# Kernel optimization log

Measured on AMD Instinct MI355X. Metric: run time of the kernel, lower is better.

The kernel has to match this reference:

```python
import jax, jax.numpy as jnp
import numpy as np

DIM = 1024
HEADS = 16
DIM_HEAD = 64
INNER = HEADS * DIM_HEAD  # 1024
SCALE = DIM_HEAD ** -0.5


def setup_inputs() -> dict:
    key = jax.random.key(0)
    k0, k1, k2 = jax.random.split(key, 3)
    x = jax.random.normal(k0, (4, 2048, DIM), dtype=jnp.float32)
    ln_gamma = jnp.ones((DIM,), dtype=jnp.float32)
    ln_beta = jnp.zeros((DIM,), dtype=jnp.float32)
    w_qkv = jax.random.normal(k1, (DIM, 3 * INNER), dtype=jnp.float32) * (DIM ** -0.5)
    w_out = jax.random.normal(k2, (INNER, DIM), dtype=jnp.float32) * (INNER ** -0.5)
    b_out = jnp.zeros((DIM,), dtype=jnp.float32)
    return {"x": x, "ln_gamma": ln_gamma, "ln_beta": ln_beta,
            "w_qkv": w_qkv, "w_out": w_out, "b_out": b_out}


def reference(x, ln_gamma, ln_beta, w_qkv, w_out, b_out):
    # LayerNorm over last dim (eps matches torch default 1e-5)
    mu = jnp.mean(x, axis=-1, keepdims=True)
    var = jnp.mean(jnp.square(x - mu), axis=-1, keepdims=True)
    xn = (x - mu) * jax.lax.rsqrt(var + 1e-5) * ln_gamma + ln_beta
    # QKV projection (no bias)
    qkv = xn @ w_qkv  # [b, t, 3*inner]
    q, k, v = jnp.split(qkv, 3, axis=-1)
    B, T, _ = x.shape
    def to_heads(t):
        return t.reshape(B, T, HEADS, DIM_HEAD).transpose(0, 2, 1, 3)  # b h t d
    q, k, v = to_heads(q), to_heads(k), to_heads(v)
    dots = jnp.einsum('bhid,bhjd->bhij', q, k) * SCALE
    attn = jax.nn.softmax(dots, axis=-1)
    out = jnp.einsum('bhij,bhjd->bhid', attn, v)
    out = out.transpose(0, 2, 1, 3).reshape(B, T, INNER)
    return out @ w_out + b_out
```

## Files before the change

kernel.cpp:

```cpp
#include <hip/hip_runtime.h>


#define DIMX 1024
#define TSEQ 2048
#define NB 4
#define NH 16
#define DH 64
#define NROWS (NB * TSEQ)
#define QSCALE 0.18033688011112042f

typedef __bf16 bf16_t;
typedef __bf16 bf16x8 __attribute__((ext_vector_type(8)));
typedef __bf16 bf16x4 __attribute__((ext_vector_type(4)));
typedef float f32x4 __attribute__((ext_vector_type(4)));

#if __has_builtin(__builtin_amdgcn_exp2f)
#define EXP2F __builtin_amdgcn_exp2f
#else
#define EXP2F exp2f
#endif

__device__ __forceinline__ bf16x4 cvt4(f32x4 v) {
    return __builtin_convertvector(v, bf16x4);
}
__device__ __forceinline__ void async16(const bf16_t* g, bf16_t* l) {
    __builtin_amdgcn_global_load_lds(
        (const __attribute__((address_space(1))) unsigned int*)g,
        (__attribute__((address_space(3))) unsigned int*)l, 16, 0, 0);
}

__global__ __launch_bounds__(256) void ln_kernel(
    const float* __restrict__ x, const float* __restrict__ g,
    const float* __restrict__ b, bf16_t* __restrict__ xn) {
    int row = blockIdx.x, tid = threadIdx.x;
    const float4 xv = *(const float4*)(x + (size_t)row * DIMX + tid * 4);
    float s = xv.x + xv.y + xv.z + xv.w;
    float q = xv.x * xv.x + xv.y * xv.y + xv.z * xv.z + xv.w * xv.w;
    for (int o = 32; o > 0; o >>= 1) {
        s += __shfl_xor(s, o);
        q += __shfl_xor(q, o);
    }
    __shared__ float2 red[4];
    int wave = tid >> 6, lane = tid & 63;
    if (lane == 0) red[wave] = make_float2(s, q);
    __syncthreads();
    float2 r0 = red[0], r1 = red[1], r2 = red[2], r3 = red[3];
    s = r0.x + r1.x + r2.x + r3.x;
    q = r0.y + r1.y + r2.y + r3.y;
    float mu = s * (1.0f / DIMX);
    float var = q * (1.0f / DIMX) - mu * mu;
    float rstd = rsqrtf(var + 1e-5f);
    float4 gv = *(const float4*)(g + tid * 4);
    float4 bv = *(const float4*)(b + tid * 4);
    f32x4 r;
    r[0] = (xv.x - mu) * rstd * gv.x + bv.x;
    r[1] = (xv.y - mu) * rstd * gv.y + bv.y;
    r[2] = (xv.z - mu) * rstd * gv.z + bv.z;
    r[3] = (xv.w - mu) * rstd * gv.w + bv.w;
    *(bf16x4*)(xn + (size_t)row * DIMX + tid * 4) = cvt4(r);
}

__global__ __launch_bounds__(256) void transpose_cast(
    const float* __restrict__ src, bf16_t* __restrict__ dst, int R, int C) {
    __shared__ float tile[32][33];
    int c0 = blockIdx.x * 32, r0 = blockIdx.y * 32;
    int tx = threadIdx.x, ty = threadIdx.y;
    for (int i = ty; i < 32; i += 8)
        tile[i][tx] = src[(size_t)(r0 + i) * C + c0 + tx];
    __syncthreads();
    for (int i = ty; i < 32; i += 8)
        dst[(size_t)(c0 + i) * R + r0 + tx] = (bf16_t)tile[tx][i];
}

#define MFMA16 __builtin_amdgcn_mfma_f32_16x16x32_bf16

template <int MODE>
__global__ __launch_bounds__(256, 2) void gemm128p(
    const bf16_t* __restrict__ A, const bf16_t* __restrict__ BT,
    void* __restrict__ Cout, const float* __restrict__ bias, int M, int N, int K) {
    __shared__ __align__(16) bf16_t As[2][128 * 64];
    __shared__ __align__(16) bf16_t Bs[2][128 * 64];
    int tid = threadIdx.x, lane = tid & 63, wave = tid >> 6;
    int lm = lane & 15, quad = lane >> 4;
    int wr = wave >> 1, wc = wave & 1;

    int nbx = gridDim.x;
    int nwg = nbx * gridDim.y;
    int linear = blockIdx.y * nbx + blockIdx.x;
    int cpx = nwg >> 3;
    int swz = (linear & 7) * cpx + (linear >> 3);
    int bx = swz % nbx, by = swz / nbx;
    int m0 = by * 128, n0 = bx * 128;

    int srow = tid >> 3, sc8 = tid & 7;
    int scol = (sc8 ^ (srow & 7)) << 3;
    const bf16_t* ga = A + (size_t)(m0 + srow) * K + scol;
    const bf16_t* gb = BT + (size_t)(n0 + srow) * K + scol;
    int ldst = tid << 3;

    int sw0 = ((quad ^ (lm & 7)) << 3);
    int sw1 = (((4 + quad) ^ (lm & 7)) << 3);

    f32x4 zero = {0.f, 0.f, 0.f, 0.f};
    f32x4 acc[4][4];
#pragma unroll
    for (int i = 0; i < 4; ++i)
#pragma unroll
        for (int j = 0; j < 4; ++j) acc[i][j] = zero;

#pragma unroll
    for (int i = 0; i < 4; ++i) async16(ga + (size_t)(i * 32) * K, &As[0][i * 2048 + ldst]);
#pragma unroll
    for (int i = 0; i < 4; ++i) async16(gb + (size_t)(i * 32) * K, &Bs[0][i * 2048 + ldst]);
    asm volatile("s_waitcnt vmcnt(0)" ::: "memory");
    __builtin_amdgcn_s_barrier();

    int nkt = K >> 6;
    for (int kt = 0; kt < nkt; ++kt) {
        int c = kt & 1;
        int k1 = (kt + 1) << 6;
        bool pf = (kt + 1) < nkt;
        const bf16_t* pa = &As[c][0];
        const bf16_t* pb = &Bs[c][0];
        bf16_t* na = &As[c ^ 1][0];
        bf16_t* nb = &Bs[c ^ 1][0];
        bf16x8 af[4][2], bfr[2][2];

#pragma unroll
        for (int t = 0; t < 4; ++t) {
            int ro = (wr * 64 + t * 16 + lm) * 64;
            af[t][0] = *(const bf16x8*)&pa[ro + sw0];
            af[t][1] = *(const bf16x8*)&pa[ro + sw1];
        }
#pragma unroll
        for (int t = 0; t < 2; ++t) {
            int ro = (wc * 64 + t * 16 + lm) * 64;
            bfr[t][0] = *(const bf16x8*)&pb[ro + sw0];
            bfr[t][1] = *(const bf16x8*)&pb[ro + sw1];
        }
        if (pf) {
#pragma unroll
            for (int i = 0; i < 4; ++i)
                async16(ga + (size_t)(i * 32) * K + k1, &na[i * 2048 + ldst]);
#pragma unroll
            for (int i = 0; i < 4; ++i)
                async16(gb + (size_t)(i * 32) * K + k1, &nb[i * 2048 + ldst]);
        }
        __builtin_amdgcn_s_barrier();
        asm volatile("s_waitcnt lgkmcnt(0)" ::: "memory");
        __builtin_amdgcn_s_setprio(1);
#pragma unroll
        for (int mt = 0; mt < 4; ++mt)
#pragma unroll
            for (int nt = 0; nt < 2; ++nt) {
                acc[mt][nt] = MFMA16(af[mt][0], bfr[nt][0], acc[mt][nt], 0, 0, 0);
                acc[mt][nt] = MFMA16(af[mt][1], bfr[nt][1], acc[mt][nt], 0, 0, 0);
            }
        __builtin_amdgcn_s_setprio(0);
        __builtin_amdgcn_s_barrier();

#pragma unroll
        for (int t = 0; t < 2; ++t) {
            int ro = (wc * 64 + (2 + t) * 16 + lm) * 64;
            bfr[t][0] = *(const bf16x8*)&pb[ro + sw0];
            bfr[t][1] = *(const bf16x8*)&pb[ro + sw1];
        }
        __builtin_amdgcn_s_barrier();
        asm volatile("s_waitcnt lgkmcnt(0)" ::: "memory");
        __builtin_amdgcn_s_setprio(1);
#pragma unroll
        for (int mt = 0; mt < 4; ++mt)
#pragma unroll
            for (int nt = 0; nt < 2; ++nt) {
                acc[mt][2 + nt] = MFMA16(af[mt][0], bfr[nt][0], acc[mt][2 + nt], 0, 0, 0);
                acc[mt][2 + nt] = MFMA16(af[mt][1], bfr[nt][1], acc[mt][2 + nt], 0, 0, 0);
            }
        __builtin_amdgcn_s_setprio(0);
        asm volatile("s_waitcnt vmcnt(0)" ::: "memory");
        __builtin_amdgcn_s_barrier();
    }

#pragma unroll
    for (int mt = 0; mt < 4; ++mt) {
#pragma unroll
        for (int nt = 0; nt < 4; ++nt) {
            int m = m0 + wr * 64 + mt * 16 + quad * 4;
            int n = n0 + wc * 64 + nt * 16 + lm;
            if (MODE == 1) {
                int sel = n >> 10, nn = n & 1023, h = nn >> 6, d = nn & 63;
                int b = m >> 11, t = m & 2047;
                if (sel == 2) {
                    *(bf16x4*)((bf16_t*)Cout + (size_t)2 * 8388608 +
                               ((size_t)((b * NH + h) * DH + d)) * TSEQ + t) = cvt4(acc[mt][nt]);
                } else {
                    f32x4 sv = acc[mt][nt] * (sel == 0 ? QSCALE : 1.0f);
                    bf16x4 c4 = cvt4(sv);
#pragma unroll
                    for (int r = 0; r < 4; ++r)
                        ((bf16_t*)Cout)[(size_t)sel * 8388608 +
                                        ((size_t)((b * NH + h) * TSEQ + t + r)) * DH + d] = c4[r];
                }
            } else {
                float bn = bias[n];
#pragma unroll
                for (int r = 0; r < 4; ++r)
                    ((float*)Cout)[(size_t)(m + r) * N + n] = acc[mt][nt][r] + bn;
            }
        }
    }
}

__global__ __launch_bounds__(512, 4) void attn_mfma(
    const bf16_t* __restrict__ qkv, bf16_t* __restrict__ o) {
    int bh = blockIdx.y;
    int qt = blockIdx.x;
    const bf16_t* qb = qkv + (size_t)bh * TSEQ * DH;
    const bf16_t* kb = qkv + (size_t)8388608 + (size_t)bh * TSEQ * DH;
    const bf16_t* vb = qkv + (size_t)16777216 + (size_t)bh * DH * TSEQ;
    int tid = threadIdx.x, wave = tid >> 6, lane = tid & 63;
    int lm = lane & 15, quad = lane >> 4, lx = lm & 7;

    __shared__ __align__(16) bf16_t Ks[2][2][64 * 64];
    __shared__ __align__(16) bf16_t Vt[2][2][64 * 64];

    int roff = tid >> 3;
    int fr = (roff & 3) | ((roff & 8) >> 1);
    int cperm = ((tid & 7) ^ fr) * 8;
    const bf16_t* kp = kb + (size_t)roff * DH + cperm;
    const bf16_t* vp = vb + (size_t)roff * TSEQ + cperm;
    int l0 = tid * 8;

    bf16x8 qf[2][2];
#pragma unroll
    for (int u = 0; u < 2; ++u)
#pragma unroll
        for (int ks = 0; ks < 2; ++ks)
            qf[u][ks] = *(const bf16x8*)(qb +
                (size_t)(qt * 256 + wave * 32 + u * 16 + lm) * DH + ks * 32 + quad * 8);

    f32x4 zero = {0.f, 0.f, 0.f, 0.f};
    f32x4 m16 = {-16.f, -16.f, -16.f, -16.f};
    f32x4 acc[2][4];
#pragma unroll
    for (int u = 0; u < 2; ++u)
#pragma unroll
        for (int dt = 0; dt < 4; ++dt) acc[u][dt] = zero;
    f32x4 l4[2] = {zero, zero};

    int qh = lm >> 2, rr = lm & 3;
    int krow0 = 8 * qh + rr;
    int krow1 = krow0 + 4;
    int krow2 = 32 + 8 * (qh ^ 2) + rr;
    int krow3 = krow2 + 4;
    int fo0 = (quad ^ lx) * 8;
    int fo1 = ((4 + quad) ^ lx) * 8;
    int fv = (lm & 3) | ((lm & 8) >> 1);
    int vo0 = (quad ^ fv) * 8;
    int vo1 = ((4 | (quad ^ 2)) ^ fv) * 8;

    async16(kp, &Ks[0][0][l0]);
    async16(kp + (size_t)64 * DH, &Ks[0][1][l0]);
    async16(vp, &Vt[0][0][l0]);
    async16(vp + 64, &Vt[0][1][l0]);
    kp += 128 * DH; vp += 128;
    asm volatile("s_waitcnt vmcnt(0)" ::: "memory");
    __builtin_amdgcn_s_barrier();

    for (int jt = 0; jt < TSEQ / 128; ++jt) {
        int c = jt & 1;
        if (jt + 1 < TSEQ / 128) {
            async16(kp, &Ks[c ^ 1][0][l0]);
            async16(kp + (size_t)64 * DH, &Ks[c ^ 1][1][l0]);
            async16(vp, &Vt[c ^ 1][0][l0]);
            async16(vp + 64, &Vt[c ^ 1][1][l0]);
            kp += 128 * DH; vp += 128;
        }

#pragma unroll
        for (int sub = 0; sub < 2; ++sub) {
            const bf16_t* Kc = &Ks[c][sub][0];
            const bf16_t* Vc = &Vt[c][sub][0];

            bf16x8 kf[4][2];
            kf[0][0] = *(const bf16x8*)&Kc[krow0 * 64 + fo0];
            kf[0][1] = *(const bf16x8*)&Kc[krow0 * 64 + fo1];
            kf[1][0] = *(const bf16x8*)&Kc[krow1 * 64 + fo0];
            kf[1][1] = *(const bf16x8*)&Kc[krow1 * 64 + fo1];
            kf[2][0] = *(const bf16x8*)&Kc[krow2 * 64 + fo0];
            kf[2][1] = *(const bf16x8*)&Kc[krow2 * 64 + fo1];
            kf[3][0] = *(const bf16x8*)&Kc[krow3 * 64 + fo0];
            kf[3][1] = *(const bf16x8*)&Kc[krow3 * 64 + fo1];

            bf16x8 pf[2][2];
#pragma unroll
            for (int u = 0; u < 2; ++u) {
                f32x4 s[4];
                __builtin_amdgcn_s_setprio(1);
#pragma unroll
                for (int nt = 0; nt < 4; ++nt) {
                    s[nt] = __builtin_amdgcn_mfma_f32_16x16x32_bf16(kf[nt][0], qf[u][0], m16, 0, 0, 0);
                    s[nt] = __builtin_amdgcn_mfma_f32_16x16x32_bf16(kf[nt][1], qf[u][1], s[nt], 0, 0, 0);
                }
                __builtin_amdgcn_s_setprio(0);
                f32x4 p[4];
#pragma unroll
                for (int nt = 0; nt < 4; ++nt) {
#pragma unroll
                    for (int e = 0; e < 4; ++e) p[nt][e] = EXP2F(s[nt][e]);
                    l4[u] += p[nt];
                }
                bf16x4 c0 = cvt4(p[0]), c1 = cvt4(p[1]), c2 = cvt4(p[2]), c3 = cvt4(p[3]);
                pf[u][0] = __builtin_shufflevector(c0, c1, 0, 1, 2, 3, 4, 5, 6, 7);
                pf[u][1] = __builtin_shufflevector(c2, c3, 0, 1, 2, 3, 4, 5, 6, 7);
            }

            __builtin_amdgcn_s_setprio(1);
#pragma unroll
            for (int dt = 0; dt < 4; ++dt) {
                bf16x8 vf0 = *(const bf16x8*)&Vc[(dt * 16 + lm) * 64 + vo0];
                bf16x8 vf1 = *(const bf16x8*)&Vc[(dt * 16 + lm) * 64 + vo1];
#pragma unroll
                for (int u = 0; u < 2; ++u) {
                    acc[u][dt] = __builtin_amdgcn_mfma_f32_16x16x32_bf16(vf0, pf[u][0], acc[u][dt], 0, 0, 0);
                    acc[u][dt] = __builtin_amdgcn_mfma_f32_16x16x32_bf16(vf1, pf[u][1], acc[u][dt], 0, 0, 0);
                }
            }
            __builtin_amdgcn_s_setprio(0);
        }

        asm volatile("s_waitcnt vmcnt(0)" ::: "memory");
        __builtin_amdgcn_s_barrier();
    }

    int b = bh >> 4, h = bh & 15;
#pragma unroll
    for (int u = 0; u < 2; ++u) {
        float l = (l4[u][0] + l4[u][1]) + (l4[u][2] + l4[u][3]);
        l += __shfl_xor(l, 16);
        l += __shfl_xor(l, 32);
        float rl = 1.0f / l;
        int t = qt * 256 + wave * 32 + u * 16 + lm;
#pragma unroll
        for (int dt = 0; dt < 4; ++dt) {
            f32x4 ov = acc[u][dt] * rl;
            *(bf16x4*)(o + ((size_t)(b * TSEQ + t)) * DIMX + h * DH + dt * 16 + quad * 4) = cvt4(ov);
        }
    }
}

extern "C" void kernel_launch(void* const* d_in, const int* in_sizes, int n_in,
                              void* d_out, int out_size, void* d_ws, size_t ws_size,
                              hipStream_t stream) {
    const float* x = (const float*)d_in[0];
    const float* g = (const float*)d_in[1];
    const float* be = (const float*)d_in[2];
    const float* w_qkv = (const float*)d_in[3];
    const float* w_out = (const float*)d_in[4];
    const float* b_out = (const float*)d_in[5];
    float* out = (float*)d_out;
    char* ws = (char*)d_ws;

    bf16_t* xn = (bf16_t*)(ws);
    bf16_t* wqkvT = (bf16_t*)(ws + 16777216);
    bf16_t* woutT = (bf16_t*)(ws + 23068672);
    bf16_t* qkv = (bf16_t*)(ws + 25165824);
    bf16_t* attno = (bf16_t*)(ws + 75497472);

    ln_kernel<<<NROWS, 256, 0, stream>>>(x, g, be, xn);
    transpose_cast<<<dim3(96, 32), dim3(32, 8), 0, stream>>>(w_qkv, wqkvT, 1024, 3072);
    transpose_cast<<<dim3(32, 32), dim3(32, 8), 0, stream>>>(w_out, woutT, 1024, 1024);
    gemm128p<1><<<dim3(24, 64), 256, 0, stream>>>(xn, wqkvT, (void*)qkv, nullptr, NROWS, 3072, 1024);
    attn_mfma<<<dim3(8, 64), 512, 0, stream>>>(qkv, attno);
    gemm128p<2><<<dim3(8, 64), 256, 0, stream>>>(attno, woutT, (void*)out, b_out, NROWS, 1024, 1024);
}
```

Baseline: 262.3 us.

## Merge LayerNorm and weight transposes into one kernel; load all B fragments at once

Fuses the LayerNorm kernel and the two weight transpose-cast kernels into a single prep kernel launch, dispatching work by block index. This removes two kernel launches and the gaps between them. In the GEMM main loop, all four B fragments are now read from LDS up front and all 16 MFMA pairs are issued in one phase. This drops the mid-iteration barriers and the second LDS read stage, at the cost of more registers held live and less interleaving of LDS reads with MFMA.

```diff
diff --git a/kernel.cpp b/kernel.cpp
--- a/kernel.cpp
+++ b/kernel.cpp
@@ -29,47 +29,58 @@
         (__attribute__((address_space(3))) unsigned int*)l, 16, 0, 0);
 }
 
-__global__ __launch_bounds__(256) void ln_kernel(
+__global__ __launch_bounds__(256) void prep_kernel(
     const float* __restrict__ x, const float* __restrict__ g,
-    const float* __restrict__ b, bf16_t* __restrict__ xn) {
-    int row = blockIdx.x, tid = threadIdx.x;
-    const float4 xv = *(const float4*)(x + (size_t)row * DIMX + tid * 4);
-    float s = xv.x + xv.y + xv.z + xv.w;
-    float q = xv.x * xv.x + xv.y * xv.y + xv.z * xv.z + xv.w * xv.w;
-    for (int o = 32; o > 0; o >>= 1) {
-        s += __shfl_xor(s, o);
-        q += __shfl_xor(q, o);
-    }
-    __shared__ float2 red[4];
-    int wave = tid >> 6, lane = tid & 63;
-    if (lane == 0) red[wave] = make_float2(s, q);
-    __syncthreads();
-    float2 r0 = red[0], r1 = red[1], r2 = red[2], r3 = red[3];
-    s = r0.x + r1.x + r2.x + r3.x;
-    q = r0.y + r1.y + r2.y + r3.y;
-    float mu = s * (1.0f / DIMX);
-    float var = q * (1.0f / DIMX) - mu * mu;
-    float rstd = rsqrtf(var + 1e-5f);
-    float4 gv = *(const float4*)(g + tid * 4);
-    float4 bv = *(const float4*)(b + tid * 4);
-    f32x4 r;
-    r[0] = (xv.x - mu) * rstd * gv.x + bv.x;
-    r[1] = (xv.y - mu) * rstd * gv.y + bv.y;
-    r[2] = (xv.z - mu) * rstd * gv.z + bv.z;
-    r[3] = (xv.w - mu) * rstd * gv.w + bv.w;
-    *(bf16x4*)(xn + (size_t)row * DIMX + tid * 4) = cvt4(r);
-}
-
-__global__ __launch_bounds__(256) void transpose_cast(
-    const float* __restrict__ src, bf16_t* __restrict__ dst, int R, int C) {
-    __shared__ float tile[32][33];
-    int c0 = blockIdx.x * 32, r0 = blockIdx.y * 32;
-    int tx = threadIdx.x, ty = threadIdx.y;
-    for (int i = ty; i < 32; i += 8)
-        tile[i][tx] = src[(size_t)(r0 + i) * C + c0 + tx];
-    __syncthreads();
-    for (int i = ty; i < 32; i += 8)
-        dst[(size_t)(c0 + i) * R + r0 + tx] = (bf16_t)tile[tx][i];
+    const float* __restrict__ b, bf16_t* __restrict__ xn,
+    const float* __restrict__ w_qkv, bf16_t* __restrict__ wqkvT,
+    const float* __restrict__ w_out, bf16_t* __restrict__ woutT) {
+    int bid = blockIdx.x, tid = threadIdx.x;
+    if (bid < NROWS) {
+        int row = bid;
+        const float4 xv = *(const float4*)(x + (size_t)row * DIMX + tid * 4);
+        float s = xv.x + xv.y + xv.z + xv.w;
+        float q = xv.x * xv.x + xv.y * xv.y + xv.z * xv.z + xv.w * xv.w;
+        for (int o = 32; o > 0; o >>= 1) {
+            s += __shfl_xor(s, o);
+            q += __shfl_xor(q, o);
+        }
+        __shared__ float2 red[4];
+        int wave = tid >> 6, lane = tid & 63;
+        if (lane == 0) red[wave] = make_float2(s, q);
+        __syncthreads();
+        float2 r0 = red[0], r1 = red[1], r2 = red[2], r3 = red[3];
+        s = r0.x + r1.x + r2.x + r3.x;
+        q = r0.y + r1.y + r2.y + r3.y;
+        float mu = s * (1.0f / DIMX);
+        float var = q * (1.0f / DIMX) - mu * mu;
+        float rstd = rsqrtf(var + 1e-5f);
+        float4 gv = *(const float4*)(g + tid * 4);
+        float4 bv = *(const float4*)(b + tid * 4);
+        f32x4 r;
+        r[0] = (xv.x - mu) * rstd * gv.x + bv.x;
+        r[1] = (xv.y - mu) * rstd * gv.y + bv.y;
+        r[2] = (xv.z - mu) * rstd * gv.z + bv.z;
+        r[3] = (xv.w - mu) * rstd * gv.w + bv.w;
+        *(bf16x4*)(xn + (size_t)row * DIMX + tid * 4) = cvt4(r);
+    } else {
+        const float* src;
+        bf16_t* dst;
+        int R, C, tb;
+        if (bid < NROWS + 3072) {
+            tb = bid - NROWS; src = w_qkv; dst = wqkvT; R = 1024; C = 3072;
+        } else {
+            tb = bid - NROWS - 3072; src = w_out; dst = woutT; R = 1024; C = 1024;
+        }
+        int ntx = C >> 5;
+        int c0 = (tb % ntx) * 32, r0 = (tb / ntx) * 32;
+        int tx = tid & 31, ty = tid >> 5;
+        __shared__ float tile[32][33];
+        for (int i = ty; i < 32; i += 8)
+            tile[i][tx] = src[(size_t)(r0 + i) * C + c0 + tx];
+        __syncthreads();
+        for (int i = ty; i < 32; i += 8)
+            dst[(size_t)(c0 + i) * R + r0 + tx] = (bf16_t)tile[tx][i];
+    }
 }
 
 #define MFMA16 __builtin_amdgcn_mfma_f32_16x16x32_bf16
@@ -124,7 +135,7 @@
         const bf16_t* pb = &Bs[c][0];
         bf16_t* na = &As[c ^ 1][0];
         bf16_t* nb = &Bs[c ^ 1][0];
-        bf16x8 af[4][2], bfr[2][2];
+        bf16x8 af[4][2], bfr[4][2];
 
 #pragma unroll
         for (int t = 0; t < 4; ++t) {
@@ -133,7 +144,7 @@
             af[t][1] = *(const bf16x8*)&pa[ro + sw1];
         }
 #pragma unroll
-        for (int t = 0; t < 2; ++t) {
+        for (int t = 0; t < 4; ++t) {
             int ro = (wc * 64 + t * 16 + lm) * 64;
             bfr[t][0] = *(const bf16x8*)&pb[ro + sw0];
             bfr[t][1] = *(const bf16x8*)&pb[ro + sw1];
@@ -146,34 +157,14 @@
             for (int i = 0; i < 4; ++i)
                 async16(gb + (size_t)(i * 32) * K + k1, &nb[i * 2048 + ldst]);
         }
-        __builtin_amdgcn_s_barrier();
         asm volatile("s_waitcnt lgkmcnt(0)" ::: "memory");
         __builtin_amdgcn_s_setprio(1);
 #pragma unroll
         for (int mt = 0; mt < 4; ++mt)
 #pragma unroll
-            for (int nt = 0; nt < 2; ++nt) {
+            for (int nt = 0; nt < 4; ++nt) {
                 acc[mt][nt] = MFMA16(af[mt][0], bfr[nt][0], acc[mt][nt], 0, 0, 0);
                 acc[mt][nt] = MFMA16(af[mt][1], bfr[nt][1], acc[mt][nt], 0, 0, 0);
-            }
-        __builtin_amdgcn_s_setprio(0);
-        __builtin_amdgcn_s_barrier();
-
-#pragma unroll
-        for (int t = 0; t < 2; ++t) {
-            int ro = (wc * 64 + (2 + t) * 16 + lm) * 64;
-            bfr[t][0] = *(const bf16x8*)&pb[ro + sw0];
-            bfr[t][1] = *(const bf16x8*)&pb[ro + sw1];
-        }
-        __builtin_amdgcn_s_barrier();
-        asm volatile("s_waitcnt lgkmcnt(0)" ::: "memory");
-        __builtin_amdgcn_s_setprio(1);
-#pragma unroll
-        for (int mt = 0; mt < 4; ++mt)
-#pragma unroll
-            for (int nt = 0; nt < 2; ++nt) {
-                acc[mt][2 + nt] = MFMA16(af[mt][0], bfr[nt][0], acc[mt][2 + nt], 0, 0, 0);
-                acc[mt][2 + nt] = MFMA16(af[mt][1], bfr[nt][1], acc[mt][2 + nt], 0, 0, 0);
             }
         __builtin_amdgcn_s_setprio(0);
         asm volatile("s_waitcnt vmcnt(0)" ::: "memory");
@@ -366,9 +357,8 @@
     bf16_t* qkv = (bf16_t*)(ws + 25165824);
     bf16_t* attno = (bf16_t*)(ws + 75497472);
 
-    ln_kernel<<<NROWS, 256, 0, stream>>>(x, g, be, xn);
-    transpose_cast<<<dim3(96, 32), dim3(32, 8), 0, stream>>>(w_qkv, wqkvT, 1024, 3072);
-    transpose_cast<<<dim3(32, 32), dim3(32, 8), 0, stream>>>(w_out, woutT, 1024, 1024);
+    prep_kernel<<<NROWS + 3072 + 1024, 256, 0, stream>>>(
+        x, g, be, xn, w_qkv, wqkvT, w_out, woutT);
     gemm128p<1><<<dim3(24, 64), 256, 0, stream>>>(xn, wqkvT, (void*)qkv, nullptr, NROWS, 3072, 1024);
     attn_mfma<<<dim3(8, 64), 512, 0, stream>>>(qkv, attno);
     gemm128p<2><<<dim3(8, 64), 256, 0, stream>>>(attno, woutT, (void*)out, b_out, NROWS, 1024, 1024);
```

Result: no change. 261.9 us (-0.2%).
